# Optimization experiments

Measured on AMD Instinct MI355X. Metric: run time of the kernel, lower is better.

The kernel has to match this reference:

```python
import jax, jax.numpy as jnp
import numpy as np

B = 65536
LAYERS = [256, 512, 512, 256]


def setup_inputs() -> dict:
    key = jax.random.key(0)
    ks = jax.random.split(key, 10)
    inp = {"data": jax.random.normal(ks[0], (B, LAYERS[0]), dtype=jnp.float32)}
    for i in range(3):
        n_in, n_out = LAYERS[i], LAYERS[i + 1]
        # link weights ~ U[0,1) like random.random(); bias params[0] zeroed in torch code
        inp[f"W{i+1}"] = jax.random.uniform(ks[1 + 3 * i], (n_in, n_out), dtype=jnp.float32)
        inp[f"b{i+1}"] = jnp.zeros((n_out,), dtype=jnp.float32)
        # per-node activation params a = params[1:6], torch.rand init
        inp[f"a{i+1}"] = jax.random.uniform(ks[2 + 3 * i], (n_out, 5), dtype=jnp.float32)
    return inp


def _act(x, a):
    # x: [B, n], a: [n, 5]; a0*tanh(x)*sin(a1*x+a2) + a3*x + a4  (per-node params broadcast over batch)
    return a[:, 0] * jnp.tanh(x) * jnp.sin(a[:, 1] * x + a[:, 2]) + a[:, 3] * x + a[:, 4]


def reference(data, W1, b1, a1, W2, b2, a2, W3, b3, a3):
    h = _act(data @ W1 + b1, a1)
    h = _act(h @ W2 + b2, a2)
    h = _act(h @ W3 + b3, a3)
    return jax.nn.softmax(h, axis=1)
```

## Files before the change

### kernel.cpp

```cpp
#include <hip/hip_runtime.h>

#define BATCH 65536

typedef float f32x4 __attribute__((ext_vector_type(4)));
typedef _Float16 f16x8 __attribute__((ext_vector_type(8)));

__device__ __forceinline__ void async_ld16(const void* g, void* l) {
  __builtin_amdgcn_global_load_lds(
      (const __attribute__((address_space(1))) void*)g,
      (__attribute__((address_space(3))) void*)l, 16, 0, 0);
}

__device__ __forceinline__ float act_f(float x, float a0, float a1, float a2,
                                       float a3, float a4) {
  float ax = fabsf(x);
  float e = __builtin_amdgcn_exp2f(ax * -2.8853900817779268f);
  float th = (1.0f - e) * __builtin_amdgcn_rcpf(1.0f + e);
  th = copysignf(th, x);
  float arg = fmaf(a1, x, a2);
  float rev = arg * 0.15915494309189535f;
  rev -= floorf(rev);
  float s = __builtin_amdgcn_sinf(rev);
  return fmaf(a3, x, fmaf(a0 * th, s, a4));
}

__global__ __launch_bounds__(256) void splitT_k(const float* __restrict__ W,
                                                _Float16* __restrict__ hi,
                                                _Float16* __restrict__ lo,
                                                int K, int N) {
  const int i = blockIdx.x * 256 + threadIdx.x;
  if (i >= K * N) return;
  const int k = i / N, n = i % N;
  const float w = W[i];
  const _Float16 h = (_Float16)w;
  hi[(size_t)n * K + k] = h;
  lo[(size_t)n * K + k] = (_Float16)(w - (float)h);
}

__device__ __forceinline__ f32x4 mfma3(f16x8 ah, f16x8 al, f16x8 bh, f16x8 bl,
                                       f32x4 c) {
  c = __builtin_amdgcn_mfma_f32_16x16x32_f16(ah, bh, c, 0, 0, 0);
  c = __builtin_amdgcn_mfma_f32_16x16x32_f16(ah, bl, c, 0, 0, 0);
  c = __builtin_amdgcn_mfma_f32_16x16x32_f16(al, bh, c, 0, 0, 0);
  return c;
}

template <bool AF32, bool FINAL>
__global__ __launch_bounds__(256, 4) void gemm_act(
    const float* __restrict__ Af, const _Float16* __restrict__ Ahi,
    const _Float16* __restrict__ Alo, const _Float16* __restrict__ Bhi,
    const _Float16* __restrict__ Blo, const float* __restrict__ bias,
    const float* __restrict__ ap, _Float16* __restrict__ Chi,
    _Float16* __restrict__ Clo, float* __restrict__ Cout, int K, int N) {
  __shared__ __align__(16) _Float16 sA[4096];
  __shared__ __align__(16) _Float16 sB[16384];

  const int tid = threadIdx.x;
  const int wv = tid >> 6;
  const int lane = tid & 63;
  const int wm = wv >> 1, wn = wv & 1;
  const int m16 = lane & 15, quad = lane >> 4;
  const int col0 = blockIdx.x * 256;
  const int row0 = blockIdx.y * 64;

  f32x4 acc[2][8];
  const f32x4 zero = {0.f, 0.f, 0.f, 0.f};
#pragma unroll
  for (int i = 0; i < 2; ++i)
#pragma unroll
    for (int j = 0; j < 8; ++j) acc[i][j] = zero;

  const int nk = K >> 5;
  for (int kt = 0; kt < nk; ++kt) {
    const int k0 = kt << 5;
    if (AF32) {
      float* sAf = (float*)sA;
#pragma unroll
      for (int t = 0; t < 2; ++t) {
        const int c = wv * 2 + t;
        const int r = c * 8 + (lane >> 3);
        const size_t ga = (size_t)(row0 + r) * K + k0 + (lane & 7) * 4;
        async_ld16(Af + ga, (void*)&sAf[c * 256]);
      }
    } else {
      const int r = wv * 16 + (lane >> 2);
      const size_t ga = (size_t)(row0 + r) * K + k0 + (lane & 3) * 8;
      async_ld16(Ahi + ga, (void*)&sA[wv * 512]);
      async_ld16(Alo + ga, (void*)&sA[2048 + wv * 512]);
    }
#pragma unroll
    for (int t = 0; t < 4; ++t) {
      const int c = wv * 4 + t;
      const int col = c * 16 + (lane >> 2);
      const size_t gb = (size_t)(col0 + col) * K + k0 + (lane & 3) * 8;
      async_ld16(Bhi + gb, (void*)&sB[c * 512]);
      async_ld16(Blo + gb, (void*)&sB[8192 + c * 512]);
    }
    __syncthreads();

    f16x8 ah[2], al[2];
#pragma unroll
    for (int tm = 0; tm < 2; ++tm) {
      const int arow = wm * 32 + tm * 16 + m16;
      if (AF32) {
        const float* pa = (const float*)sA + arow * 32 + quad * 8;
        const f32x4 x0 = *(const f32x4*)pa;
        const f32x4 x1 = *(const f32x4*)(pa + 4);
#pragma unroll
        for (int j = 0; j < 4; ++j) {
          const _Float16 h0 = (_Float16)x0[j];
          ah[tm][j] = h0;
          al[tm][j] = (_Float16)(x0[j] - (float)h0);
          const _Float16 h1 = (_Float16)x1[j];
          ah[tm][4 + j] = h1;
          al[tm][4 + j] = (_Float16)(x1[j] - (float)h1);
        }
      } else {
        ah[tm] = *(const f16x8*)&sA[arow * 32 + quad * 8];
        al[tm] = *(const f16x8*)&sA[2048 + arow * 32 + quad * 8];
      }
    }
#pragma unroll
    for (int tn = 0; tn < 8; ++tn) {
      const int bcol = wn * 128 + tn * 16 + m16;
      const f16x8 bh = *(const f16x8*)&sB[bcol * 32 + quad * 8];
      const f16x8 bl = *(const f16x8*)&sB[8192 + bcol * 32 + quad * 8];
#pragma unroll
      for (int tm = 0; tm < 2; ++tm)
        acc[tm][tn] = mfma3(ah[tm], al[tm], bh, bl, acc[tm][tn]);
    }
    __syncthreads();
  }

#pragma unroll
  for (int tn = 0; tn < 8; ++tn) {
    const int col = col0 + wn * 128 + tn * 16 + m16;
    const float bs = bias[col];
    const float p0 = ap[col * 5 + 0];
    const float p1 = ap[col * 5 + 1];
    const float p2 = ap[col * 5 + 2];
    const float p3 = ap[col * 5 + 3];
    const float p4 = ap[col * 5 + 4];
#pragma unroll
    for (int tm = 0; tm < 2; ++tm) {
      const int row = row0 + wm * 32 + tm * 16 + quad * 4;
#pragma unroll
      for (int r = 0; r < 4; ++r) {
        const float y = act_f(acc[tm][tn][r] + bs, p0, p1, p2, p3, p4);
        if (FINAL) {
          Cout[(size_t)(row + r) * 256 + col] = y;
        } else {
          const size_t o = (size_t)(row + r) * N + col;
          const _Float16 h = (_Float16)y;
          Chi[o] = h;
          Clo[o] = (_Float16)(y - (float)h);
        }
      }
    }
  }
}

__global__ __launch_bounds__(256) void softmax_rows(float* __restrict__ io) {
  const int wv = threadIdx.x >> 6, lane = threadIdx.x & 63;
  const size_t row = (size_t)blockIdx.x * 4 + wv;
  f32x4* p = (f32x4*)(io + row * 256);
  f32x4 v = p[lane];
  float m = fmaxf(fmaxf(v[0], v[1]), fmaxf(v[2], v[3]));
#pragma unroll
  for (int off = 32; off > 0; off >>= 1) m = fmaxf(m, __shfl_xor(m, off));
  f32x4 e;
  float s = 0.f;
#pragma unroll
  for (int j = 0; j < 4; ++j) {
    e[j] = __builtin_amdgcn_exp2f((v[j] - m) * 1.4426950408889634f);
    s += e[j];
  }
#pragma unroll
  for (int off = 32; off > 0; off >>= 1) s += __shfl_xor(s, off);
  const float inv = __builtin_amdgcn_rcpf(s);
#pragma unroll
  for (int j = 0; j < 4; ++j) e[j] *= inv;
  p[lane] = e;
}

extern "C" void kernel_launch(void* const* d_in, const int* in_sizes, int n_in,
                              void* d_out, int out_size, void* d_ws,
                              size_t ws_size, hipStream_t stream) {
  const float* data = (const float*)d_in[0];
  const float* W1 = (const float*)d_in[1];
  const float* b1 = (const float*)d_in[2];
  const float* a1 = (const float*)d_in[3];
  const float* W2 = (const float*)d_in[4];
  const float* b2 = (const float*)d_in[5];
  const float* a2 = (const float*)d_in[6];
  const float* W3 = (const float*)d_in[7];
  const float* b3 = (const float*)d_in[8];
  const float* a3 = (const float*)d_in[9];
  float* out = (float*)d_out;

  char* ws = (char*)d_ws;
  const size_t KB = 1024, MB = 1024 * 1024;
  _Float16* w1hi = (_Float16*)(ws + 0 * KB);
  _Float16* w1lo = (_Float16*)(ws + 256 * KB);
  _Float16* w2hi = (_Float16*)(ws + 512 * KB);
  _Float16* w2lo = (_Float16*)(ws + 1024 * KB);
  _Float16* w3hi = (_Float16*)(ws + 1536 * KB);
  _Float16* w3lo = (_Float16*)(ws + 1792 * KB);
  _Float16* h1hi = (_Float16*)(ws + 2 * MB);
  _Float16* h1lo = (_Float16*)(ws + 2 * MB + (size_t)BATCH * 512 * 2);
  _Float16* h2lo = (_Float16*)(ws + 2 * MB + (size_t)BATCH * 512 * 4);
  _Float16* h2hi = (_Float16*)d_out;

  splitT_k<<<(256 * 512 + 255) / 256, 256, 0, stream>>>(W1, w1hi, w1lo, 256, 512);
  splitT_k<<<(512 * 512 + 255) / 256, 256, 0, stream>>>(W2, w2hi, w2lo, 512, 512);
  splitT_k<<<(512 * 256 + 255) / 256, 256, 0, stream>>>(W3, w3hi, w3lo, 512, 256);

  gemm_act<true, false><<<dim3(2, BATCH / 64), 256, 0, stream>>>(
      data, nullptr, nullptr, w1hi, w1lo, b1, a1, h1hi, h1lo, nullptr, 256, 512);
  gemm_act<false, false><<<dim3(2, BATCH / 64), 256, 0, stream>>>(
      nullptr, h1hi, h1lo, w2hi, w2lo, b2, a2, h2hi, h2lo, nullptr, 512, 512);
  gemm_act<false, true><<<dim3(1, BATCH / 64), 256, 0, stream>>>(
      nullptr, h2hi, h2lo, w3hi, w3lo, b3, a3, nullptr, nullptr, out, 512, 256);

  softmax_rows<<<BATCH / 4, 256, 0, stream>>>(out);
}
```

Baseline: 438.9 us.

## Enlarge GEMM row tile, swizzle LDS layout, fuse softmax into final GEMM

Doubles the per-block row tile from 64 to 128 rows, giving each wave a 4x8 accumulator tile, and lowers launch bounds to 2 blocks per SM. Adds XOR swizzling to the LDS staging layout to reduce bank conflicts on fragment reads. Fuses the row softmax into the last GEMM epilogue, using cross-lane shuffles and an LDS exchange between the two column halves, and drops the separate softmax kernel and its extra pass over the output. The larger tile raises register and LDS use, which lowers occupancy.

Measured after the change: 442.5 us. Within noise of the previous version (+0.8%).

```diff
diff --git a/kernel.cpp b/kernel.cpp
--- a/kernel.cpp
+++ b/kernel.cpp
@@ -46,13 +46,13 @@
 }
 
 template <bool AF32, bool FINAL>
-__global__ __launch_bounds__(256, 4) void gemm_act(
+__global__ __launch_bounds__(256, 2) void gemm_act(
     const float* __restrict__ Af, const _Float16* __restrict__ Ahi,
     const _Float16* __restrict__ Alo, const _Float16* __restrict__ Bhi,
     const _Float16* __restrict__ Blo, const float* __restrict__ bias,
     const float* __restrict__ ap, _Float16* __restrict__ Chi,
     _Float16* __restrict__ Clo, float* __restrict__ Cout, int K, int N) {
-  __shared__ __align__(16) _Float16 sA[4096];
+  __shared__ __align__(16) _Float16 sA[8192];
   __shared__ __align__(16) _Float16 sB[16384];
 
   const int tid = threadIdx.x;
@@ -61,12 +61,19 @@
   const int wm = wv >> 1, wn = wv & 1;
   const int m16 = lane & 15, quad = lane >> 4;
   const int col0 = blockIdx.x * 256;
-  const int row0 = blockIdx.y * 64;
-
-  f32x4 acc[2][8];
+  const int row0 = blockIdx.y * 128;
+
+  const int rl4 = lane >> 2, sl4 = lane & 3;
+  const int sg4 = sl4 ^ ((rl4 >> 1) & 3);
+  const int rl8 = lane >> 3, sl8 = lane & 7;
+  const int sg8 = sl8 ^ rl8;
+  const int fswz = (quad ^ ((m16 >> 1) & 3)) * 8;
+  const int rc7 = m16 & 7;
+
+  f32x4 acc[4][8];
   const f32x4 zero = {0.f, 0.f, 0.f, 0.f};
 #pragma unroll
-  for (int i = 0; i < 2; ++i)
+  for (int i = 0; i < 4; ++i)
 #pragma unroll
     for (int j = 0; j < 8; ++j) acc[i][j] = zero;
 
@@ -76,36 +83,37 @@
     if (AF32) {
       float* sAf = (float*)sA;
 #pragma unroll
+      for (int t = 0; t < 4; ++t) {
+        const int c = wv * 4 + t;
+        const size_t ga = (size_t)(row0 + c * 8 + rl8) * K + k0 + sg8 * 4;
+        async_ld16(Af + ga, (void*)&sAf[c * 256]);
+      }
+    } else {
+#pragma unroll
       for (int t = 0; t < 2; ++t) {
         const int c = wv * 2 + t;
-        const int r = c * 8 + (lane >> 3);
-        const size_t ga = (size_t)(row0 + r) * K + k0 + (lane & 7) * 4;
-        async_ld16(Af + ga, (void*)&sAf[c * 256]);
-      }
-    } else {
-      const int r = wv * 16 + (lane >> 2);
-      const size_t ga = (size_t)(row0 + r) * K + k0 + (lane & 3) * 8;
-      async_ld16(Ahi + ga, (void*)&sA[wv * 512]);
-      async_ld16(Alo + ga, (void*)&sA[2048 + wv * 512]);
+        const size_t ga = (size_t)(row0 + c * 16 + rl4) * K + k0 + sg4 * 8;
+        async_ld16(Ahi + ga, (void*)&sA[c * 512]);
+        async_ld16(Alo + ga, (void*)&sA[4096 + c * 512]);
+      }
     }
 #pragma unroll
     for (int t = 0; t < 4; ++t) {
       const int c = wv * 4 + t;
-      const int col = c * 16 + (lane >> 2);
-      const size_t gb = (size_t)(col0 + col) * K + k0 + (lane & 3) * 8;
+      const size_t gb = (size_t)(col0 + c * 16 + rl4) * K + k0 + sg4 * 8;
       async_ld16(Bhi + gb, (void*)&sB[c * 512]);
       async_ld16(Blo + gb, (void*)&sB[8192 + c * 512]);
     }
     __syncthreads();
 
-    f16x8 ah[2], al[2];
-#pragma unroll
-    for (int tm = 0; tm < 2; ++tm) {
-      const int arow = wm * 32 + tm * 16 + m16;
+    f16x8 ah[4], al[4];
+#pragma unroll
+    for (int tm = 0; tm < 4; ++tm) {
       if (AF32) {
-        const float* pa = (const float*)sA + arow * 32 + quad * 8;
-        const f32x4 x0 = *(const f32x4*)pa;
-        const f32x4 x1 = *(const f32x4*)(pa + 4);
+        const int chunk = wm * 8 + tm * 2 + (m16 >> 3);
+        const float* sAf = (const float*)sA + chunk * 256 + rc7 * 32;
+        const f32x4 x0 = *(const f32x4*)(sAf + ((2 * quad) ^ rc7) * 4);
+        const f32x4 x1 = *(const f32x4*)(sAf + ((2 * quad + 1) ^ rc7) * 4);
 #pragma unroll
         for (int j = 0; j < 4; ++j) {
           const _Float16 h0 = (_Float16)x0[j];
@@ -116,40 +124,39 @@
           al[tm][4 + j] = (_Float16)(x1[j] - (float)h1);
         }
       } else {
-        ah[tm] = *(const f16x8*)&sA[arow * 32 + quad * 8];
-        al[tm] = *(const f16x8*)&sA[2048 + arow * 32 + quad * 8];
-      }
-    }
-#pragma unroll
-    for (int tn = 0; tn < 8; ++tn) {
-      const int bcol = wn * 128 + tn * 16 + m16;
-      const f16x8 bh = *(const f16x8*)&sB[bcol * 32 + quad * 8];
-      const f16x8 bl = *(const f16x8*)&sB[8192 + bcol * 32 + quad * 8];
-#pragma unroll
-      for (int tm = 0; tm < 2; ++tm)
+        const int idx = (wm * 4 + tm) * 512 + m16 * 32 + fswz;
+        ah[tm] = *(const f16x8*)&sA[idx];
+        al[tm] = *(const f16x8*)&sA[4096 + idx];
+      }
+    }
+#pragma unroll
+    for (int tn = 0; tn < 8; ++tn) {
+      const int idx = (wn * 8 + tn) * 512 + m16 * 32 + fswz;
+      const f16x8 bh = *(const f16x8*)&sB[idx];
+      const f16x8 bl = *(const f16x8*)&sB[8192 + idx];
+#pragma unroll
+      for (int tm = 0; tm < 4; ++tm)
         acc[tm][tn] = mfma3(ah[tm], al[tm], bh, bl, acc[tm][tn]);
     }
     __syncthreads();
   }
 
-#pragma unroll
-  for (int tn = 0; tn < 8; ++tn) {
-    const int col = col0 + wn * 128 + tn * 16 + m16;
-    const float bs = bias[col];
-    const float p0 = ap[col * 5 + 0];
-    const float p1 = ap[col * 5 + 1];
-    const float p2 = ap[col * 5 + 2];
-    const float p3 = ap[col * 5 + 3];
-    const float p4 = ap[col * 5 + 4];
-#pragma unroll
-    for (int tm = 0; tm < 2; ++tm) {
-      const int row = row0 + wm * 32 + tm * 16 + quad * 4;
-#pragma unroll
-      for (int r = 0; r < 4; ++r) {
-        const float y = act_f(acc[tm][tn][r] + bs, p0, p1, p2, p3, p4);
-        if (FINAL) {
-          Cout[(size_t)(row + r) * 256 + col] = y;
-        } else {
+  if (!FINAL) {
+#pragma unroll
+    for (int tn = 0; tn < 8; ++tn) {
+      const int col = col0 + wn * 128 + tn * 16 + m16;
+      const float bs = bias[col];
+      const float p0 = ap[col * 5 + 0];
+      const float p1 = ap[col * 5 + 1];
+      const float p2 = ap[col * 5 + 2];
+      const float p3 = ap[col * 5 + 3];
+      const float p4 = ap[col * 5 + 4];
+#pragma unroll
+      for (int tm = 0; tm < 4; ++tm) {
+        const int row = row0 + wm * 64 + tm * 16 + quad * 4;
+#pragma unroll
+        for (int r = 0; r < 4; ++r) {
+          const float y = act_f(acc[tm][tn][r] + bs, p0, p1, p2, p3, p4);
           const size_t o = (size_t)(row + r) * N + col;
           const _Float16 h = (_Float16)y;
           Chi[o] = h;
@@ -157,30 +164,89 @@
         }
       }
     }
+  } else {
+    const float L2E = 1.4426950408889634f;
+    float mx[16], sm[16];
+#pragma unroll
+    for (int i = 0; i < 16; ++i) mx[i] = -1e30f;
+#pragma unroll
+    for (int tn = 0; tn < 8; ++tn) {
+      const int col = wn * 128 + tn * 16 + m16;
+      const float bs = bias[col];
+      const float p0 = ap[col * 5 + 0];
+      const float p1 = ap[col * 5 + 1];
+      const float p2 = ap[col * 5 + 2];
+      const float p3 = ap[col * 5 + 3];
+      const float p4 = ap[col * 5 + 4];
+#pragma unroll
+      for (int tm = 0; tm < 4; ++tm)
+#pragma unroll
+        for (int r = 0; r < 4; ++r) {
+          const float y = act_f(acc[tm][tn][r] + bs, p0, p1, p2, p3, p4);
+          acc[tm][tn][r] = y;
+          mx[tm * 4 + r] = fmaxf(mx[tm * 4 + r], y);
+        }
+    }
+#pragma unroll
+    for (int i = 0; i < 16; ++i)
+#pragma unroll
+      for (int off = 1; off < 16; off <<= 1)
+        mx[i] = fmaxf(mx[i], __shfl_xor(mx[i], off));
+#pragma unroll
+    for (int i = 0; i < 16; ++i) sm[i] = 0.f;
+#pragma unroll
+    for (int tn = 0; tn < 8; ++tn)
+#pragma unroll
+      for (int tm = 0; tm < 4; ++tm)
+#pragma unroll
+        for (int r = 0; r < 4; ++r) {
+          const float e = __builtin_amdgcn_exp2f(
+              (acc[tm][tn][r] - mx[tm * 4 + r]) * L2E);
+          acc[tm][tn][r] = e;
+          sm[tm * 4 + r] += e;
+        }
+#pragma unroll
+    for (int i = 0; i < 16; ++i)
+#pragma unroll
+      for (int off = 1; off < 16; off <<= 1) sm[i] += __shfl_xor(sm[i], off);
+    float* part = (float*)sA;
+    if (m16 == 0) {
+#pragma unroll
+      for (int tm = 0; tm < 4; ++tm)
+#pragma unroll
+        for (int r = 0; r < 4; ++r) {
+          const int row = wm * 64 + tm * 16 + quad * 4 + r;
+          part[(wn * 128 + row) * 2 + 0] = mx[tm * 4 + r];
+          part[(wn * 128 + row) * 2 + 1] = sm[tm * 4 + r];
+        }
+    }
+    __syncthreads();
+    float sc[16];
+#pragma unroll
+    for (int tm = 0; tm < 4; ++tm)
+#pragma unroll
+      for (int r = 0; r < 4; ++r) {
+        const int i = tm * 4 + r;
+        const int row = wm * 64 + tm * 16 + quad * 4 + r;
+        const float mo = part[((1 - wn) * 128 + row) * 2 + 0];
+        const float so = part[((1 - wn) * 128 + row) * 2 + 1];
+        const float M = fmaxf(mx[i], mo);
+        const float a = __builtin_amdgcn_exp2f((mx[i] - M) * L2E);
+        const float b = __builtin_amdgcn_exp2f((mo - M) * L2E);
+        sc[i] = a * __builtin_amdgcn_rcpf(fmaf(sm[i], a, so * b));
+      }
+#pragma unroll
+    for (int tn = 0; tn < 8; ++tn) {
+      const int col = wn * 128 + tn * 16 + m16;
+#pragma unroll
+      for (int tm = 0; tm < 4; ++tm) {
+        const int row = row0 + wm * 64 + tm * 16 + quad * 4;
+#pragma unroll
+        for (int r = 0; r < 4; ++r)
+          Cout[(size_t)(row + r) * 256 + col] = acc[tm][tn][r] * sc[tm * 4 + r];
+      }
+    }
   }
-}
-
-__global__ __launch_bounds__(256) void softmax_rows(float* __restrict__ io) {
-  const int wv = threadIdx.x >> 6, lane = threadIdx.x & 63;
-  const size_t row = (size_t)blockIdx.x * 4 + wv;
-  f32x4* p = (f32x4*)(io + row * 256);
-  f32x4 v = p[lane];
-  float m = fmaxf(fmaxf(v[0], v[1]), fmaxf(v[2], v[3]));
-#pragma unroll
-  for (int off = 32; off > 0; off >>= 1) m = fmaxf(m, __shfl_xor(m, off));
-  f32x4 e;
-  float s = 0.f;
-#pragma unroll
-  for (int j = 0; j < 4; ++j) {
-    e[j] = __builtin_amdgcn_exp2f((v[j] - m) * 1.4426950408889634f);
-    s += e[j];
-  }
-#pragma unroll
-  for (int off = 32; off > 0; off >>= 1) s += __shfl_xor(s, off);
-  const float inv = __builtin_amdgcn_rcpf(s);
-#pragma unroll
-  for (int j = 0; j < 4; ++j) e[j] *= inv;
-  p[lane] = e;
 }
 
 extern "C" void kernel_launch(void* const* d_in, const int* in_sizes, int n_in,
@@ -215,12 +281,10 @@
   splitT_k<<<(512 * 512 + 255) / 256, 256, 0, stream>>>(W2, w2hi, w2lo, 512, 512);
   splitT_k<<<(512 * 256 + 255) / 256, 256, 0, stream>>>(W3, w3hi, w3lo, 512, 256);
 
-  gemm_act<true, false><<<dim3(2, BATCH / 64), 256, 0, stream>>>(
+  gemm_act<true, false><<<dim3(2, BATCH / 128), 256, 0, stream>>>(
       data, nullptr, nullptr, w1hi, w1lo, b1, a1, h1hi, h1lo, nullptr, 256, 512);
-  gemm_act<false, false><<<dim3(2, BATCH / 64), 256, 0, stream>>>(
+  gemm_act<false, false><<<dim3(2, BATCH / 128), 256, 0, stream>>>(
       nullptr, h1hi, h1lo, w2hi, w2lo, b2, a2, h2hi, h2lo, nullptr, 512, 512);
-  gemm_act<false, true><<<dim3(1, BATCH / 64), 256, 0, stream>>>(
+  gemm_act<false, true><<<dim3(1, BATCH / 128), 256, 0, stream>>>(
       nullptr, h2hi, h2lo, w3hi, w3lo, b3, a3, nullptr, nullptr, out, 512, 256);
-
-  softmax_rows<<<BATCH / 4, 256, 0, stream>>>(out);
-}
+}
```
